# Optimization experiments

Measured on AMD Instinct MI355X. Metric: run time of the kernel, lower is better.

Reference implementation:

```python
import jax, jax.numpy as jnp
import numpy as np

D_MODEL = 512
SRC_LEN = 256
TGT_LEN = 256
EPS = 1e-8


def setup_inputs() -> dict:
    key = jax.random.key(0)
    k1, k2, k3, k4, k5, k6 = jax.random.split(key, 6)
    B = 8
    dec = jax.random.normal(k1, (B, TGT_LEN, D_MODEL), dtype=jnp.float32)
    enc = jax.random.normal(k2, (B, SRC_LEN, D_MODEL), dtype=jnp.float32)
    input_lengths = jax.random.randint(k3, (B,), 1, SRC_LEN + 1)
    # torch Linear(d_model, src_length) weights, stored transposed for x @ W
    s = 1.0 / np.sqrt(D_MODEL)
    W1 = jax.random.uniform(k4, (D_MODEL, SRC_LEN), minval=-s, maxval=s, dtype=jnp.float32)
    W2 = jax.random.uniform(k5, (D_MODEL, SRC_LEN), minval=-s, maxval=s, dtype=jnp.float32)
    sv = 1.0 / np.sqrt(SRC_LEN)
    vt = jax.random.uniform(k6, (SRC_LEN,), minval=-sv, maxval=sv, dtype=jnp.float32)
    return {"decoder_hidden_states": dec, "encoder_hidden_states": enc,
            "input_lengths": input_lengths, "W1": W1, "W2": W2, "vt": vt}


def reference(decoder_hidden_states, encoder_hidden_states, input_lengths, W1, W2, vt):
    B, src, _ = encoder_hidden_states.shape
    dt = jnp.einsum('btd,dl->btl', decoder_hidden_states, W1)   # [B,tgt,L]
    et = jnp.einsum('bsd,dl->bsl', encoder_hidden_states, W2)   # [B,src,L]
    # [B,tgt,src,L] broadcast add + tanh, reduced by vt -> [B,tgt,src]
    scores = jnp.einsum('btsl,l->bts', jnp.tanh(dt[:, :, None, :] + et[:, None, :, :]), vt)
    mask = (jnp.arange(src) < input_lengths[:, None])[:, None, :]  # [B,1,src]
    scores = scores + jnp.log(mask.astype(scores.dtype) + EPS)
    log_score = jax.nn.log_softmax(scores, axis=-1)             # over src
    return jnp.swapaxes(log_score, -1, -2)                      # [B,src,tgt]
```

## Files before the change

### kernel.cpp

```cpp
#include <hip/hip_runtime.h>
#include <hip/hip_bf16.h>

#define TGT 256
#define SRC 256
#define LDIM 256
#define DM 512
#define BATCH 8

#define C2LOG2E 2.8853902f
#define LOG2E 1.4426950f
#define LN2 0.6931472f
#define LOGEPS -18.420681f

#if __has_builtin(__builtin_amdgcn_exp2f)
#define EXP2F(x) __builtin_amdgcn_exp2f(x)
#else
#define EXP2F(x) exp2f(x)
#endif
#if __has_builtin(__builtin_amdgcn_rcpf)
#define RCPF(x) __builtin_amdgcn_rcpf(x)
#else
#define RCPF(x) (1.0f / (x))
#endif
#if __has_builtin(__builtin_amdgcn_logf)
#define LOG2F_(x) __builtin_amdgcn_logf(x)
#else
#define LOG2F_(x) __log2f(x)
#endif

typedef short bf16x8 __attribute__((ext_vector_type(8)));
typedef float f32x4 __attribute__((ext_vector_type(4)));

__device__ __forceinline__ unsigned int f2b_pk(float lo, float hi) {
    union { float f; unsigned int u; } a, b;
    a.f = lo; b.f = hi;
    unsigned int ra = (a.u + 0x7fffu + ((a.u >> 16) & 1u)) >> 16;
    unsigned int rb = (b.u + 0x7fffu + ((b.u >> 16) & 1u)) >> 16;
    return (ra & 0xffffu) | (rb << 16);
}

__global__ __launch_bounds__(256) void wtrans_k(
    const float* __restrict__ W1, const float* __restrict__ W2,
    unsigned short* __restrict__ Wt)
{
    __shared__ float tile[32][33];
    const int mat = blockIdx.z;
    const float* __restrict__ W = mat ? W2 : W1;
    unsigned short* __restrict__ dst = Wt + (size_t)mat * LDIM * DM;
    const int k0 = blockIdx.x * 32, n0 = blockIdx.y * 32;
    const int tx = threadIdx.x & 31, ty = threadIdx.x >> 5;
    #pragma unroll
    for (int i = 0; i < 32; i += 8)
        tile[ty + i][tx] = W[(size_t)(k0 + ty + i) * LDIM + n0 + tx];
    __syncthreads();
    #pragma unroll
    for (int i = 0; i < 32; i += 8) {
        union { float f; unsigned int u; } v; v.f = tile[tx][ty + i];
        dst[(size_t)(n0 + ty + i) * DM + k0 + tx] =
            (unsigned short)((v.u + 0x7fffu + ((v.u >> 16) & 1u)) >> 16);
    }
}

#define APITCH 72

__global__ __launch_bounds__(512) void gemm_k(
    const float* __restrict__ dec, const float* __restrict__ enc,
    const unsigned short* __restrict__ Wt, float* __restrict__ E)
{
    __shared__ unsigned short As[64 * APITCH];
    __shared__ unsigned short Bs[64 * APITCH];

    const int tid = threadIdx.x;
    const int m0 = blockIdx.y * 64;
    const int n0 = blockIdx.x * 64;
    const bool is_dec = (m0 < 2048);
    const float* __restrict__ X = is_dec ? dec : enc;
    const unsigned short* __restrict__ Wm = Wt + (is_dec ? 0 : (size_t)LDIM * DM);
    const int xr0 = is_dec ? m0 : m0 - 2048;

    const int arow = tid >> 3;
    const int aoff = (tid & 7) << 3;
    const float* __restrict__ aptr = X + (size_t)(xr0 + arow) * DM + aoff;
    const unsigned short* __restrict__ bptr = Wm + (size_t)(n0 + arow) * DM + aoff;

    const int wave = tid >> 6;
    const int lane = tid & 63;
    const int l15 = lane & 15;
    const int quad = lane >> 4;
    const int wm = wave >> 1;
    const int wn = wave & 1;

    f32x4 acc[2] = {};
    float4 a0, a1;
    uint4 bb;

    a0 = *(const float4*)(aptr + 0);
    a1 = *(const float4*)(aptr + 4);
    bb = *(const uint4*)(bptr);

    for (int it = 0; it < DM / 64; ++it) {
        if (it) __syncthreads();
        uint4 wa;
        wa.x = f2b_pk(a0.x, a0.y); wa.y = f2b_pk(a0.z, a0.w);
        wa.z = f2b_pk(a1.x, a1.y); wa.w = f2b_pk(a1.z, a1.w);
        *(uint4*)&As[arow * APITCH + aoff] = wa;
        *(uint4*)&Bs[arow * APITCH + aoff] = bb;
        __syncthreads();
        if (it < DM / 64 - 1) {
            const int ko = (it + 1) * 64;
            a0 = *(const float4*)(aptr + ko + 0);
            a1 = *(const float4*)(aptr + ko + 4);
            bb = *(const uint4*)(bptr + ko);
        }
        #pragma unroll
        for (int kb = 0; kb < 64; kb += 32) {
            const bf16x8 af = *(const bf16x8*)&As[(wm * 16 + l15) * APITCH + kb + quad * 8];
            #pragma unroll
            for (int c = 0; c < 2; ++c) {
                const bf16x8 bf = *(const bf16x8*)&Bs[(wn * 32 + c * 16 + l15) * APITCH + kb + quad * 8];
                acc[c] = __builtin_amdgcn_mfma_f32_16x16x32_bf16(af, bf, acc[c], 0, 0, 0);
            }
        }
    }

    const int orow = m0 + wm * 16 + quad * 4;
    const int ocol = n0 + wn * 32 + l15;
    #pragma unroll
    for (int c = 0; c < 2; ++c)
        #pragma unroll
        for (int r = 0; r < 4; ++r)
            E[(size_t)(orow + r) * LDIM + ocol + c * 16] = EXP2F(acc[c][r] * C2LOG2E);
}

__device__ __forceinline__ void pair_acc(
    const float4 d0, const float4 d1, const float e0, const float e1,
    const float v0, const float v1, float4& acc)
{
    float4 p0, p1, num, den;
    p0.x = fmaf(d0.x, e0, 1.f); p0.y = fmaf(d0.y, e0, 1.f);
    p0.z = fmaf(d0.z, e0, 1.f); p0.w = fmaf(d0.w, e0, 1.f);
    p1.x = fmaf(d1.x, e1, 1.f); p1.y = fmaf(d1.y, e1, 1.f);
    p1.z = fmaf(d1.z, e1, 1.f); p1.w = fmaf(d1.w, e1, 1.f);
    num.x = fmaf(v1, p0.x, v0 * p1.x); num.y = fmaf(v1, p0.y, v0 * p1.y);
    num.z = fmaf(v1, p0.z, v0 * p1.z); num.w = fmaf(v1, p0.w, v0 * p1.w);
    den.x = p0.x * p1.x; den.y = p0.y * p1.y;
    den.z = p0.z * p1.z; den.w = p0.w * p1.w;
    acc.x = fmaf(num.x, RCPF(den.x), acc.x);
    acc.y = fmaf(num.y, RCPF(den.y), acc.y);
    acc.z = fmaf(num.z, RCPF(den.z), acc.z);
    acc.w = fmaf(num.w, RCPF(den.w), acc.w);
}

__global__ __launch_bounds__(512) void scores_k(
    const float* __restrict__ E, const int* __restrict__ lens,
    const float* __restrict__ vt, float* __restrict__ out)
{
    __shared__ __align__(16) float dtr[LDIM][4];
    __shared__ __align__(16) float vt2s[LDIM];
    __shared__ __align__(16) float4 accs[256];
    __shared__ float4 wred[4];

    const int tid = threadIdx.x;
    const int s = tid & 255;
    const int h = tid >> 8;
    const int b = blockIdx.y;
    const int t0 = blockIdx.x * 4;
    const float* __restrict__ Ed = E;
    const float* __restrict__ Ee = E + (size_t)2048 * LDIM;

    #pragma unroll
    for (int i = h; i < 4; i += 2)
        dtr[s][i] = Ed[(size_t)(b * TGT + t0 + i) * LDIM + s];
    if (tid < 256) vt2s[tid] = -2.0f * vt[tid];
    __syncthreads();

    float4 acc = {0.f, 0.f, 0.f, 0.f};
    const float* __restrict__ erow = Ee + (size_t)(b * SRC + s) * LDIM;

    const int lbase = h * 128;
    for (int l0 = lbase; l0 < lbase + 128; l0 += 4) {
        const float4 e4 = *(const float4*)(erow + l0);
        const float4 v4 = *(const float4*)&vt2s[l0];
        const float4 d0 = *(const float4*)&dtr[l0 + 0][0];
        const float4 d1 = *(const float4*)&dtr[l0 + 1][0];
        const float4 d2 = *(const float4*)&dtr[l0 + 2][0];
        const float4 d3 = *(const float4*)&dtr[l0 + 3][0];
        pair_acc(d0, d1, e4.x, e4.y, v4.x, v4.y, acc);
        pair_acc(d2, d3, e4.z, e4.w, v4.z, v4.w, acc);
    }

    if (h == 1) accs[s] = acc;
    __syncthreads();

    const int wid = tid >> 6, lane = tid & 63;
    float4 mx, sm;

    if (h == 0) {
        const float4 o4 = accs[s];
        acc.x += o4.x; acc.y += o4.y; acc.z += o4.z; acc.w += o4.w;
        const float madd = (s < lens[b]) ? 0.0f : LOGEPS;
        acc.x += madd; acc.y += madd; acc.z += madd; acc.w += madd;

        float4 r = acc;
        #pragma unroll
        for (int off = 32; off > 0; off >>= 1) {
            r.x = fmaxf(r.x, __shfl_down(r.x, off));
            r.y = fmaxf(r.y, __shfl_down(r.y, off));
            r.z = fmaxf(r.z, __shfl_down(r.z, off));
            r.w = fmaxf(r.w, __shfl_down(r.w, off));
        }
        if (lane == 0) wred[wid] = r;
    }
    __syncthreads();

    if (h == 0) {
        mx = wred[0];
        #pragma unroll
        for (int w = 1; w < 4; ++w) {
            mx.x = fmaxf(mx.x, wred[w].x);
            mx.y = fmaxf(mx.y, wred[w].y);
            mx.z = fmaxf(mx.z, wred[w].z);
            mx.w = fmaxf(mx.w, wred[w].w);
        }
    }
    __syncthreads();

    if (h == 0) {
        float4 ex;
        ex.x = EXP2F((acc.x - mx.x) * LOG2E);
        ex.y = EXP2F((acc.y - mx.y) * LOG2E);
        ex.z = EXP2F((acc.z - mx.z) * LOG2E);
        ex.w = EXP2F((acc.w - mx.w) * LOG2E);
        float4 sr = ex;
        #pragma unroll
        for (int off = 32; off > 0; off >>= 1) {
            sr.x += __shfl_down(sr.x, off);
            sr.y += __shfl_down(sr.y, off);
            sr.z += __shfl_down(sr.z, off);
            sr.w += __shfl_down(sr.w, off);
        }
        if (lane == 0) wred[wid] = sr;
    }
    __syncthreads();

    if (h == 0) {
        sm = wred[0];
        #pragma unroll
        for (int w = 1; w < 4; ++w) {
            sm.x += wred[w].x; sm.y += wred[w].y; sm.z += wred[w].z; sm.w += wred[w].w;
        }
        float4 o;
        o.x = acc.x - (mx.x + LOG2F_(sm.x) * LN2);
        o.y = acc.y - (mx.y + LOG2F_(sm.y) * LN2);
        o.z = acc.z - (mx.z + LOG2F_(sm.z) * LN2);
        o.w = acc.w - (mx.w + LOG2F_(sm.w) * LN2);
        *(float4*)(out + (size_t)(b * SRC + s) * TGT + t0) = o;
    }
}

extern "C" void kernel_launch(void* const* d_in, const int* in_sizes, int n_in,
                              void* d_out, int out_size, void* d_ws, size_t ws_size,
                              hipStream_t stream) {
    const float* dec = (const float*)d_in[0];
    const float* enc = (const float*)d_in[1];
    const int* lens  = (const int*)d_in[2];
    const float* W1  = (const float*)d_in[3];
    const float* W2  = (const float*)d_in[4];
    const float* vt  = (const float*)d_in[5];
    float* out = (float*)d_out;

    unsigned short* Wt = (unsigned short*)d_ws;
    float* E = (float*)((char*)d_ws + (size_t)2 * LDIM * DM * sizeof(unsigned short));

    wtrans_k<<<dim3(16, 8, 2), 256, 0, stream>>>(W1, W2, Wt);
    gemm_k<<<dim3(LDIM / 64, 4096 / 64), 512, 0, stream>>>(dec, enc, Wt, E);
    scores_k<<<dim3(TGT / 4, BATCH), 512, 0, stream>>>(E, lens, vt, out);
}
```

Before: 98.12 us.

## Deepen GEMM K-step to 128 and remap block IDs for batch-interleaved scheduling

The GEMM now stages 128-wide K slices per iteration with a fully unrolled four-step loop, halving the number of barrier/store phases. Block IDs for both the GEMM and scores kernels are flattened and remapped so consecutive blocks cycle over the batch index, likely to spread work across XCDs/L2 slices so each batch's E rows stay cache-local. Costs include doubled LDS per tile (wider pitch), more registers for prefetch, and possibly lower occupancy.

```diff
diff --git a/kernel.cpp b/kernel.cpp
--- a/kernel.cpp
+++ b/kernel.cpp
@@ -61,7 +61,7 @@
     }
 }
 
-#define APITCH 72
+#define APITCH 136
 
 __global__ __launch_bounds__(512) void gemm_k(
     const float* __restrict__ dec, const float* __restrict__ enc,
@@ -71,15 +71,21 @@
     __shared__ unsigned short Bs[64 * APITCH];
 
     const int tid = threadIdx.x;
-    const int m0 = blockIdx.y * 64;
-    const int n0 = blockIdx.x * 64;
-    const bool is_dec = (m0 < 2048);
+    const int bid = blockIdx.x;
+    const int b    = bid & 7;
+    const int j    = bid >> 3;
+    const int mt   = j & 3;
+    const int n0   = ((j >> 2) & 3) * 64;
+    const int part = j >> 4;
+    const int m0 = part * 2048 + b * 256 + mt * 64;
+
+    const bool is_dec = (part == 0);
     const float* __restrict__ X = is_dec ? dec : enc;
     const unsigned short* __restrict__ Wm = Wt + (is_dec ? 0 : (size_t)LDIM * DM);
-    const int xr0 = is_dec ? m0 : m0 - 2048;
+    const int xr0 = b * 256 + mt * 64;
 
     const int arow = tid >> 3;
-    const int aoff = (tid & 7) << 3;
+    const int aoff = (tid & 7) << 4;
     const float* __restrict__ aptr = X + (size_t)(xr0 + arow) * DM + aoff;
     const unsigned short* __restrict__ bptr = Wm + (size_t)(n0 + arow) * DM + aoff;
 
@@ -91,29 +97,40 @@
     const int wn = wave & 1;
 
     f32x4 acc[2] = {};
-    float4 a0, a1;
-    uint4 bb;
+    float4 a0, a1, a2, a3;
+    uint4 bb0, bb1;
 
     a0 = *(const float4*)(aptr + 0);
     a1 = *(const float4*)(aptr + 4);
-    bb = *(const uint4*)(bptr);
-
-    for (int it = 0; it < DM / 64; ++it) {
+    a2 = *(const float4*)(aptr + 8);
+    a3 = *(const float4*)(aptr + 12);
+    bb0 = *(const uint4*)(bptr + 0);
+    bb1 = *(const uint4*)(bptr + 8);
+
+    #pragma unroll
+    for (int it = 0; it < DM / 128; ++it) {
         if (it) __syncthreads();
-        uint4 wa;
-        wa.x = f2b_pk(a0.x, a0.y); wa.y = f2b_pk(a0.z, a0.w);
-        wa.z = f2b_pk(a1.x, a1.y); wa.w = f2b_pk(a1.z, a1.w);
-        *(uint4*)&As[arow * APITCH + aoff] = wa;
-        *(uint4*)&Bs[arow * APITCH + aoff] = bb;
+        uint4 wa0, wa1;
+        wa0.x = f2b_pk(a0.x, a0.y); wa0.y = f2b_pk(a0.z, a0.w);
+        wa0.z = f2b_pk(a1.x, a1.y); wa0.w = f2b_pk(a1.z, a1.w);
+        wa1.x = f2b_pk(a2.x, a2.y); wa1.y = f2b_pk(a2.z, a2.w);
+        wa1.z = f2b_pk(a3.x, a3.y); wa1.w = f2b_pk(a3.z, a3.w);
+        *(uint4*)&As[arow * APITCH + aoff]     = wa0;
+        *(uint4*)&As[arow * APITCH + aoff + 8] = wa1;
+        *(uint4*)&Bs[arow * APITCH + aoff]     = bb0;
+        *(uint4*)&Bs[arow * APITCH + aoff + 8] = bb1;
         __syncthreads();
-        if (it < DM / 64 - 1) {
-            const int ko = (it + 1) * 64;
+        if (it < DM / 128 - 1) {
+            const int ko = (it + 1) * 128;
             a0 = *(const float4*)(aptr + ko + 0);
             a1 = *(const float4*)(aptr + ko + 4);
-            bb = *(const uint4*)(bptr + ko);
-        }
-        #pragma unroll
-        for (int kb = 0; kb < 64; kb += 32) {
+            a2 = *(const float4*)(aptr + ko + 8);
+            a3 = *(const float4*)(aptr + ko + 12);
+            bb0 = *(const uint4*)(bptr + ko + 0);
+            bb1 = *(const uint4*)(bptr + ko + 8);
+        }
+        #pragma unroll
+        for (int kb = 0; kb < 128; kb += 32) {
             const bf16x8 af = *(const bf16x8*)&As[(wm * 16 + l15) * APITCH + kb + quad * 8];
             #pragma unroll
             for (int c = 0; c < 2; ++c) {
@@ -163,8 +180,8 @@
     const int tid = threadIdx.x;
     const int s = tid & 255;
     const int h = tid >> 8;
-    const int b = blockIdx.y;
-    const int t0 = blockIdx.x * 4;
+    const int b = blockIdx.x & 7;
+    const int t0 = (blockIdx.x >> 3) * 4;
     const float* __restrict__ Ed = E;
     const float* __restrict__ Ee = E + (size_t)2048 * LDIM;
 
@@ -273,6 +290,6 @@
     float* E = (float*)((char*)d_ws + (size_t)2 * LDIM * DM * sizeof(unsigned short));
 
     wtrans_k<<<dim3(16, 8, 2), 256, 0, stream>>>(W1, W2, Wt);
-    gemm_k<<<dim3(LDIM / 64, 4096 / 64), 512, 0, stream>>>(dec, enc, Wt, E);
-    scores_k<<<dim3(TGT / 4, BATCH), 512, 0, stream>>>(E, lens, vt, out);
-}
+    gemm_k<<<256, 512, 0, stream>>>(dec, enc, Wt, E);
+    scores_k<<<512, 512, 0, stream>>>(E, lens, vt, out);
+}
```

Result: faster. 94.59 us (-3.6%).
